# Performance work log

Hardware: AMD Instinct MI355X
Metric: run time of the kernel (lower is better)

The kernel has to match this reference:

```python
import jax, jax.numpy as jnp
import numpy as np

B, T, D = 32, 512, 384
DUR_MAX = 8                 # durations drawn in [0, DUR_MAX)
MAX_OUT = T * (DUR_MAX - 1) # static upper bound on total expanded length (3584)
ALPHA = 1.0


def setup_inputs() -> dict:
    key = jax.random.key(0)
    k1, k2 = jax.random.split(key)
    x = jax.random.normal(k1, (B, T, D), dtype=jnp.float32)
    durations = jax.random.randint(k2, (B, T), 0, DUR_MAX, dtype=jnp.int32)
    return {"input": x, "durations": durations}


def reference(input, durations):
    # patched_dur = clamp(round(alpha * dur), min=0)
    patched = jnp.round(ALPHA * durations.astype(jnp.float32)).astype(jnp.int32)
    patched = jnp.maximum(patched, 0)                       # [B, T]
    cum = jnp.cumsum(patched, axis=1)                       # [B, T] exclusive-right boundaries
    total = cum[:, -1:]                                      # [B, 1] true expanded lengths

    pos = jnp.arange(MAX_OUT, dtype=jnp.int32)               # [MAX_OUT]
    # output frame j comes from token idx = first t with cum[t] > j
    idx = jax.vmap(lambda c: jnp.searchsorted(c, pos, side='right'))(cum)  # [B, MAX_OUT]
    idx = jnp.clip(idx, 0, T - 1)
    valid = pos[None, :] < total                              # [B, MAX_OUT]

    out = jnp.take_along_axis(input, idx[:, :, None], axis=1)  # [B, MAX_OUT, D]
    return jnp.where(valid[:, :, None], out, jnp.zeros((), dtype=input.dtype))
```

## Files before the change

kernel.cpp:

```cpp
#include <hip/hip_runtime.h>

typedef float v4f __attribute__((ext_vector_type(4)));

#define NB 32
#define NT 512
#define ND 384
#define MAX_OUT 3584
#define NV (ND / 4)
#define TPR (NV / 2)
#define BLK 256

__global__ __launch_bounds__(NT) void lr_scan_scatter(
    const int* __restrict__ dur, int* __restrict__ totals, int* __restrict__ idxmap)
{
    __shared__ int s[NT];
    const int b = blockIdx.x;
    const int t = threadIdx.x;

    int d = dur[b * NT + t];
    d = d > 0 ? d : 0;
    s[t] = d;
    __syncthreads();

    #pragma unroll
    for (int off = 1; off < NT; off <<= 1) {
        int v = (t >= off) ? s[t - off] : 0;
        __syncthreads();
        s[t] += v;
        __syncthreads();
    }
    const int cum = s[t];
    const int start = cum - d;

    int* base = idxmap + b * MAX_OUT;
    for (int j = 0; j < d; ++j) base[start + j] = t;

    if (t == NT - 1) totals[b] = cum;
}

__global__ __launch_bounds__(BLK) void lr_gather2(
    const v4f* __restrict__ in, const int* __restrict__ totals,
    const int* __restrict__ idxmap, v4f* __restrict__ out)
{
    const unsigned g8 = gridDim.x >> 3;
    const unsigned nb = (blockIdx.x & 7u) * g8 + (blockIdx.x >> 3);
    const unsigned g  = nb * BLK + threadIdx.x;

    const unsigned row = g / TPR;
    const unsigned col = g - row * TPR;
    const unsigned b   = row / MAX_OUT;
    const unsigned pos = row - b * MAX_OUT;

    const int tot = totals[b];
    const int idx = idxmap[row];

    v4f r0 = {0.f, 0.f, 0.f, 0.f};
    v4f r1 = {0.f, 0.f, 0.f, 0.f};
    if ((int)pos < tot) {
        const v4f* src = in + (unsigned)(b * NT + idx) * NV + col * 2u;
        r0 = src[0];
        r1 = src[1];
    }
    v4f* dst = out + (size_t)g * 2u;
    __builtin_nontemporal_store(r0, dst);
    __builtin_nontemporal_store(r1, dst + 1);
}

extern "C" void kernel_launch(void* const* d_in, const int* in_sizes, int n_in,
                              void* d_out, int out_size, void* d_ws, size_t ws_size,
                              hipStream_t stream)
{
    const float* x   = (const float*)d_in[0];
    const int*   dur = (const int*)d_in[1];

    int* totals = (int*)d_ws;
    int* idxmap = (int*)((char*)d_ws + 128);

    lr_scan_scatter<<<NB, NT, 0, stream>>>(dur, totals, idxmap);

    const unsigned n_thr = (unsigned)NB * MAX_OUT * TPR;
    lr_gather2<<<n_thr / BLK, BLK, 0, stream>>>(
        (const v4f*)x, totals, idxmap, (v4f*)d_out);
}
```

Before: 216.2 us.

## Tile gather by 64-row blocks with shared index cache and wave-shuffle scan

```diff
diff --git a/kernel.cpp b/kernel.cpp
--- a/kernel.cpp
+++ b/kernel.cpp
@@ -6,30 +6,36 @@
 #define NT 512
 #define ND 384
 #define MAX_OUT 3584
-#define NV (ND / 4)
-#define TPR (NV / 2)
+#define NV 96
+#define TILE 64
 #define BLK 256
+#define PER (TILE * NV / BLK)
+#define TILES_PER_B (MAX_OUT / TILE)
 
 __global__ __launch_bounds__(NT) void lr_scan_scatter(
     const int* __restrict__ dur, int* __restrict__ totals, int* __restrict__ idxmap)
 {
-    __shared__ int s[NT];
+    __shared__ int wsum[NT / 64];
     const int b = blockIdx.x;
     const int t = threadIdx.x;
+    const int lane = t & 63;
+    const int w = t >> 6;
 
     int d = dur[b * NT + t];
     d = d > 0 ? d : 0;
-    s[t] = d;
+
+    int c = d;
+    #pragma unroll
+    for (int off = 1; off < 64; off <<= 1) {
+        int v = __shfl_up(c, off, 64);
+        if (lane >= off) c += v;
+    }
+    if (lane == 63) wsum[w] = c;
     __syncthreads();
 
-    #pragma unroll
-    for (int off = 1; off < NT; off <<= 1) {
-        int v = (t >= off) ? s[t - off] : 0;
-        __syncthreads();
-        s[t] += v;
-        __syncthreads();
-    }
-    const int cum = s[t];
+    int add = 0;
+    for (int i = 0; i < w; ++i) add += wsum[i];
+    const int cum = c + add;
     const int start = cum - d;
 
     int* base = idxmap + b * MAX_OUT;
@@ -38,32 +44,53 @@
     if (t == NT - 1) totals[b] = cum;
 }
 
-__global__ __launch_bounds__(BLK) void lr_gather2(
+__global__ __launch_bounds__(BLK) void lr_gather(
     const v4f* __restrict__ in, const int* __restrict__ totals,
     const int* __restrict__ idxmap, v4f* __restrict__ out)
 {
     const unsigned g8 = gridDim.x >> 3;
-    const unsigned nb = (blockIdx.x & 7u) * g8 + (blockIdx.x >> 3);
-    const unsigned g  = nb * BLK + threadIdx.x;
+    const unsigned blk = (blockIdx.x & 7u) * g8 + (blockIdx.x >> 3);
 
-    const unsigned row = g / TPR;
-    const unsigned col = g - row * TPR;
-    const unsigned b   = row / MAX_OUT;
-    const unsigned pos = row - b * MAX_OUT;
+    const unsigned b    = blk / TILES_PER_B;
+    const unsigned tile = blk - b * TILES_PER_B;
+    const unsigned row0 = tile * TILE;
 
-    const int tot = totals[b];
-    const int idx = idxmap[row];
+    __shared__ int sidx[TILE];
+    __shared__ int stot;
+    const int t = threadIdx.x;
+    if (t < TILE) sidx[t] = idxmap[b * MAX_OUT + row0 + t];
+    if (t == 0)   stot = totals[b];
+    __syncthreads();
 
-    v4f r0 = {0.f, 0.f, 0.f, 0.f};
-    v4f r1 = {0.f, 0.f, 0.f, 0.f};
-    if ((int)pos < tot) {
-        const v4f* src = in + (unsigned)(b * NT + idx) * NV + col * 2u;
-        r0 = src[0];
-        r1 = src[1];
+    const int nvalid = stot - (int)row0;
+    const v4f* inb  = in  + (size_t)b * NT * NV;
+    v4f*       outb = out + ((size_t)b * MAX_OUT + row0) * NV;
+
+    if (nvalid >= TILE) {
+        #pragma unroll
+        for (int k = 0; k < PER; ++k) {
+            const int i = t + k * BLK;
+            const int r = i / NV;
+            const int c = i - r * NV;
+            const v4f v = inb[sidx[r] * NV + c];
+            __builtin_nontemporal_store(v, outb + i);
+        }
+    } else if (nvalid <= 0) {
+        const v4f z = {0.f, 0.f, 0.f, 0.f};
+        #pragma unroll
+        for (int k = 0; k < PER; ++k)
+            __builtin_nontemporal_store(z, outb + t + k * BLK);
+    } else {
+        #pragma unroll
+        for (int k = 0; k < PER; ++k) {
+            const int i = t + k * BLK;
+            const int r = i / NV;
+            const int c = i - r * NV;
+            v4f v = {0.f, 0.f, 0.f, 0.f};
+            if (r < nvalid) v = inb[sidx[r] * NV + c];
+            __builtin_nontemporal_store(v, outb + i);
+        }
     }
-    v4f* dst = out + (size_t)g * 2u;
-    __builtin_nontemporal_store(r0, dst);
-    __builtin_nontemporal_store(r1, dst + 1);
 }
 
 extern "C" void kernel_launch(void* const* d_in, const int* in_sizes, int n_in,
@@ -78,7 +105,7 @@
 
     lr_scan_scatter<<<NB, NT, 0, stream>>>(dur, totals, idxmap);
 
-    const unsigned n_thr = (unsigned)NB * MAX_OUT * TPR;
-    lr_gather2<<<n_thr / BLK, BLK, 0, stream>>>(
+    const unsigned n_blk = (unsigned)NB * TILES_PER_B;
+    lr_gather<<<n_blk, BLK, 0, stream>>>(
         (const v4f*)x, totals, idxmap, (v4f*)d_out);
 }
```

Measured after the change: 207.7 us. 3.9% less time.
